# Performance work log

Measured on AMD Instinct MI355X. Metric: run time of the kernel, lower is better.

The kernel has to match this reference:

```python
import jax, jax.numpy as jnp
import numpy as np

K = 10  # hardcoded top-k in the original forward


def setup_inputs() -> dict:
    key = jax.random.key(0)
    ks = jax.random.split(key, 7)
    B, F, N = 192, 256, 512
    stdv = 1.0 / np.sqrt(F)
    return {
        "v": jax.random.normal(ks[0], (B, F, N), dtype=jnp.float32),
        "g_w": jax.random.normal(ks[1], (F, F), dtype=jnp.float32) * stdv,  # Conv1d k=1 weight [out,in]
        "g_b": jax.random.normal(ks[2], (F,), dtype=jnp.float32) * stdv,
        "w1": jax.random.uniform(ks[3], (F, F), jnp.float32, -stdv, stdv),
        "b1": jax.random.uniform(ks[4], (F,), jnp.float32, -stdv, stdv),
        "w2": jax.random.uniform(ks[5], (F, F), jnp.float32, -stdv, stdv),
        "b2": jax.random.uniform(ks[6], (F,), jnp.float32, -stdv, stdv),
    }


def reference(v, g_w, g_b, w1, b1, w2, b2):
    B, Fdim, N = v.shape
    # g: Conv1d(k=1) then permute -> [B, N, nhid]
    g_v = jnp.einsum('bfn,hf->bnh', v, g_w) + g_b
    # affinity A = v^T v : [B, N, N]
    A = jnp.einsum('bfn,bfm->bnm', v, v)
    # top-K sparsification: keep only top-K entries per row
    _, idx = jax.lax.top_k(A, K)  # [B, N, K]
    b_i = jnp.arange(B)[:, None, None]
    n_i = jnp.arange(N)[None, :, None]
    keep = jnp.zeros(A.shape, dtype=bool).at[b_i, n_i, idx].set(True)
    A = jnp.where(keep, A, jnp.zeros((), A.dtype))
    # add self loops
    A = A + jnp.eye(N, dtype=A.dtype)
    # D^-0.5 A D^-0.5 (diagonal scaling, equivalent to diag_embed matmuls)
    deg = jnp.sum(A, axis=-1)  # [B, N]
    d = deg ** -0.5
    d = jnp.where(jnp.isinf(d), jnp.zeros((), d.dtype), d)
    A_hat = d[:, :, None] * A * d[:, None, :]
    # GCN layer 1: relu(A_hat @ (g_v @ w1) + b1)  (dropout p=0 -> identity)
    x = jax.nn.relu(jnp.einsum('bnm,bmh->bnh', A_hat, g_v @ w1) + b1)
    # GCN layer 2
    x = jnp.einsum('bnm,bmh->bnh', A_hat, x @ w2) + b2
    # permute back and residual
    return jnp.transpose(x, (0, 2, 1)) + v
```

## Files before the change

kernel.cpp:

```cpp
#include <hip/hip_runtime.h>
#include <float.h>

#define F_DIM 256
#define N_DIM 512
#define B_DIM 192
#define K_TOP 10

typedef __attribute__((ext_vector_type(8))) short short8;
typedef __attribute__((ext_vector_type(4))) float f32x4;

__device__ inline unsigned short f2bf(float x) {
    unsigned u = __builtin_bit_cast(unsigned, x);
    return (unsigned short)((u + 0x7fffu + ((u >> 16) & 1u)) >> 16);
}

__global__ __launch_bounds__(256) void k_combine(const float* __restrict__ g_w,
                                                 const float* __restrict__ g_b,
                                                 const float* __restrict__ w1,
                                                 const float* __restrict__ w2,
                                                 unsigned short* __restrict__ Wt1,
                                                 float* __restrict__ bc,
                                                 unsigned short* __restrict__ W2t) {
    const int j = threadIdx.x;
    const int bx = blockIdx.x;
    if (bx < F_DIM) {
        float acc = 0.f;
        for (int h = 0; h < F_DIM; ++h) acc += g_w[h * F_DIM + bx] * w1[h * F_DIM + j];
        Wt1[j * F_DIM + bx] = f2bf(acc);
    } else if (bx == F_DIM) {
        float acc = 0.f;
        for (int h = 0; h < F_DIM; ++h) acc += g_b[h] * w1[h * F_DIM + j];
        bc[j] = acc;
    } else {
        int f = bx - F_DIM - 1;
        W2t[j * F_DIM + f] = f2bf(w2[f * F_DIM + j]);
    }
}

__global__ __launch_bounds__(256) void k_to_bf16t(const float* __restrict__ v,
                                                  unsigned short* __restrict__ vt) {
    __shared__ float tile[32][33];
    const int b = blockIdx.z;
    const int n0 = blockIdx.x * 32;
    const int f0 = blockIdx.y * 32;
    const int tx = threadIdx.x & 31, ty = threadIdx.x >> 5;
    const float* vb = v + (size_t)b * F_DIM * N_DIM;
#pragma unroll
    for (int q = 0; q < 4; ++q)
        tile[ty + q * 8][tx] = vb[(size_t)(f0 + ty + q * 8) * N_DIM + n0 + tx];
    __syncthreads();
    const int wn = threadIdx.x >> 4;
    const int wf = threadIdx.x & 15;
    unsigned* vt32 = (unsigned*)vt;
#pragma unroll
    for (int q2 = 0; q2 < 2; ++q2) {
        int row = wn + q2 * 16;
        unsigned lo = f2bf(tile[wf * 2][row]);
        unsigned hi = f2bf(tile[wf * 2 + 1][row]);
        vt32[(size_t)(b * N_DIM + n0 + row) * (F_DIM / 2) + (f0 >> 1) + wf] = lo | (hi << 16);
    }
}

__global__ __launch_bounds__(256, 2) void k_topk_reg(const unsigned short* __restrict__ vt,
                                                     float* __restrict__ deg,
                                                     int* __restrict__ idxb,
                                                     float* __restrict__ wb) {
    __shared__ unsigned short stage[2][N_DIM * 32];

    const int lid = blockIdx.y * 8 + blockIdx.x;
    const int slot = lid >> 3;
    const int b = (lid & 7) + 8 * (slot >> 3);
    const int nblk = slot & 7;

    const int w = threadIdx.x >> 6;
    const int l = threadIdx.x & 63;
    const int l15 = l & 15;
    const int g = l >> 4;
    const int n0w = nblk * 64 + w * 16;
    const unsigned short* vtb = vt + (size_t)b * N_DIM * F_DIM;

    short8 bf[8];
#pragma unroll
    for (int s = 0; s < 8; ++s)
        bf[s] = *(const short8*)(vtb + (size_t)(n0w + l15) * F_DIM + s * 32 + g * 8);

    f32x4 acc[32];
#pragma unroll
    for (int mt = 0; mt < 32; ++mt) acc[mt] = (f32x4){0.f, 0.f, 0.f, 0.f};

#define STAGE(c, bufi)                                                           \
    {                                                                            \
        _Pragma("unroll")                                                        \
        for (int k = 0; k < 8; ++k) {                                            \
            int sid = w * 512 + k * 64 + l;                                      \
            int row = sid >> 2;                                                  \
            int sl = sid & 3;                                                    \
            const unsigned short* src = vtb + (size_t)row * F_DIM + (c) * 32 +   \
                                        ((sl ^ ((row >> 1) & 3)) << 3);          \
            __builtin_amdgcn_global_load_lds(                                    \
                (const __attribute__((address_space(1))) void*)src,              \
                (__attribute__((address_space(3))) void*)(                       \
                    (char*)&stage[bufi][0] + (size_t)(w * 512 + k * 64) * 16),   \
                16, 0, 0);                                                       \
        }                                                                        \
    }

    STAGE(0, 0);
    asm volatile("s_waitcnt vmcnt(0)" ::: "memory");
    __syncthreads();

    const int slx = g ^ ((l15 >> 1) & 3);
    for (int c = 0; c < 8; ++c) {
        const int cur = c & 1;
        if (c < 7) STAGE(c + 1, cur ^ 1);
        const char* sb = (const char*)&stage[cur][0];
        short8 bcur = bf[c];
#pragma unroll
        for (int mt = 0; mt < 32; ++mt) {
            const int row = mt * 16 + l15;
            short8 a = *(const short8*)(sb + row * 64 + (slx << 4));
            acc[mt] = __builtin_amdgcn_mfma_f32_16x16x32_bf16(a, bcur, acc[mt], 0, 0, 0);
        }
        asm volatile("s_waitcnt vmcnt(0)" ::: "memory");
        __syncthreads();
    }
#undef STAGE

    const int row = b * N_DIM + n0w + l15;
    float sum = 0.f;
    for (int it = 0; it < K_TOP; ++it) {
        float chv[4]; int che[4];
#pragma unroll
        for (int c = 0; c < 4; ++c) {
            float tv[16]; int te[16];
#pragma unroll
            for (int p = 0; p < 16; ++p) {
                const int e0 = c * 32 + 2 * p, e1 = e0 + 1;
                float a = acc[e0 >> 2][e0 & 3];
                float bb2 = acc[e1 >> 2][e1 & 3];
                bool tk = bb2 > a;
                tv[p] = tk ? bb2 : a;
                te[p] = tk ? e1 : e0;
            }
#pragma unroll
            for (int len = 8; len >= 1; len >>= 1) {
#pragma unroll
                for (int i2 = 0; i2 < 8; ++i2) {
                    if (i2 < len) {
                        bool tk = tv[i2 + len] > tv[i2];
                        tv[i2] = tk ? tv[i2 + len] : tv[i2];
                        te[i2] = tk ? te[i2 + len] : te[i2];
                    }
                }
            }
            chv[c] = tv[0]; che[c] = te[0];
        }
        bool t1 = chv[1] > chv[0];
        float m0 = t1 ? chv[1] : chv[0]; int ea = t1 ? che[1] : che[0];
        bool t2 = chv[3] > chv[2];
        float m1 = t2 ? chv[3] : chv[2]; int eb = t2 ? che[3] : che[2];
        bool t3 = m1 > m0;
        float bv = t3 ? m1 : m0; int be = t3 ? eb : ea;
        int bm = ((be >> 2) << 4) | (g << 2) | (be & 3);

#pragma unroll
        for (int off = 16; off <= 32; off <<= 1) {
            float ov = __shfl_xor(bv, off, 64);
            int om = __shfl_xor(bm, off, 64);
            if (ov > bv || (ov == bv && om < bm)) { bv = ov; bm = om; }
        }
        sum += bv;
        if (l < 16) {
            idxb[row * K_TOP + it] = bm;
            wb[row * (K_TOP + 1) + it] = bv;
        }
        if (it < K_TOP - 1) {
            int eo = ((bm >> 4) << 2) | (bm & 3);
            eo = (((bm >> 2) & 3) == g) ? eo : 999;
#pragma unroll
            for (int e = 0; e < 128; ++e)
                acc[e >> 2][e & 3] = (e == eo) ? -FLT_MAX : acc[e >> 2][e & 3];
        }
    }
    if (l < 16) deg[row] = sum + 1.0f;
}

template <bool ADD_BIAS>
__global__ __launch_bounds__(256, 2) void k_gemm_mfma(const unsigned short* __restrict__ At,
                                                      const unsigned short* __restrict__ Wt,
                                                      const float* __restrict__ bias,
                                                      float* __restrict__ C) {
    const int b = blockIdx.y;
    const int w = threadIdx.x >> 6;
    const int l = threadIdx.x & 63;
    const int l15 = l & 15;
    const int g = l >> 4;
    const int n0w = blockIdx.x * 128 + w * 32;
    const unsigned short* Ab = At + (size_t)b * N_DIM * F_DIM;

    f32x4 acc0[16], acc1[16];
#pragma unroll
    for (int jt = 0; jt < 16; ++jt) {
        acc0[jt] = (f32x4){0.f, 0.f, 0.f, 0.f};
        acc1[jt] = (f32x4){0.f, 0.f, 0.f, 0.f};
    }

    for (int s = 0; s < 8; ++s) {
        short8 a0 = *(const short8*)(Ab + (size_t)(n0w + l15) * F_DIM + s * 32 + g * 8);
        short8 a1 = *(const short8*)(Ab + (size_t)(n0w + 16 + l15) * F_DIM + s * 32 + g * 8);
#pragma unroll
        for (int jt = 0; jt < 16; ++jt) {
            short8 bf = *(const short8*)(Wt + (size_t)(jt * 16 + l15) * F_DIM + s * 32 + g * 8);
            acc0[jt] = __builtin_amdgcn_mfma_f32_16x16x32_bf16(a0, bf, acc0[jt], 0, 0, 0);
            acc1[jt] = __builtin_amdgcn_mfma_f32_16x16x32_bf16(a1, bf, acc1[jt], 0, 0, 0);
        }
    }

#pragma unroll
    for (int jt = 0; jt < 16; ++jt) {
        float bv = ADD_BIAS ? bias[jt * 16 + l15] : 0.f;
#pragma unroll
        for (int q = 0; q < 4; ++q) {
            int r0 = n0w + g * 4 + q;
            C[((size_t)b * N_DIM + r0) * F_DIM + jt * 16 + l15] = acc0[jt][q] + bv;
            int r1 = n0w + 16 + g * 4 + q;
            C[((size_t)b * N_DIM + r1) * F_DIM + jt * 16 + l15] = acc1[jt][q] + bv;
        }
    }
}

__global__ __launch_bounds__(256) void k_spmm_bf16(const float* __restrict__ X,
                                                   const int* __restrict__ idxb,
                                                   const float* __restrict__ wbr,
                                                   const float* __restrict__ deg,
                                                   const float* __restrict__ bias,
                                                   unsigned short* __restrict__ Y) {
    const int lid = blockIdx.x;
    const int slot = lid >> 3;
    const int b = (lid & 7) + 8 * (slot >> 7);
    const int rowblk = slot & 127;
    const int w = threadIdx.x >> 6;
    const int l = threadIdx.x & 63;
    const int row = b * N_DIM + rowblk * 4 + w;

    const float* Xb = X + ((size_t)b << 9) * F_DIM;
    const float* degb = deg + b * N_DIM;
    const int* id = idxb + row * K_TOP;
    const float* raw = wbr + row * (K_TOP + 1);

    const float dgs = deg[row];
    const float dn = (dgs == 0.f) ? 0.f : 1.f / sqrtf(dgs);
    float4 bv = ((const float4*)bias)[l];
    float4 xv = ((const float4*)(X + (size_t)row * F_DIM))[l];
    const float ws = dn * dn;
    float4 acc;
    acc.x = ws * xv.x + bv.x; acc.y = ws * xv.y + bv.y;
    acc.z = ws * xv.z + bv.z; acc.w = ws * xv.w + bv.w;
#pragma unroll
    for (int i = 0; i < K_TOP; ++i) {
        int m = id[i];
        float dgm = degb[m];
        float dm = (dgm == 0.f) ? 0.f : 1.f / sqrtf(dgm);
        float wi = dn * raw[i] * dm;
        float4 gv = ((const float4*)(Xb + ((size_t)m << 8)))[l];
        acc.x += wi * gv.x; acc.y += wi * gv.y;
        acc.z += wi * gv.z; acc.w += wi * gv.w;
    }
    acc.x = fmaxf(acc.x, 0.f); acc.y = fmaxf(acc.y, 0.f);
    acc.z = fmaxf(acc.z, 0.f); acc.w = fmaxf(acc.w, 0.f);
    uint2 p;
    p.x = (unsigned)f2bf(acc.x) | ((unsigned)f2bf(acc.y) << 16);
    p.y = (unsigned)f2bf(acc.z) | ((unsigned)f2bf(acc.w) << 16);
    ((uint2*)Y)[(size_t)row * (F_DIM / 4) + l] = p;
}

__global__ __launch_bounds__(256) void k_spmm_trans(const float* __restrict__ X,
                                                    const int* __restrict__ idxb,
                                                    const float* __restrict__ wbr,
                                                    const float* __restrict__ deg,
                                                    const float* __restrict__ bias,
                                                    const float* __restrict__ v,
                                                    float* __restrict__ out) {
    __shared__ float tile[32][257];
    const int lid = blockIdx.x;
    const int slot = lid >> 3;
    const int b = (lid & 7) + 8 * (slot >> 4);
    const int n0 = (slot & 15) * 32;
    const int w = threadIdx.x >> 6;
    const int l = threadIdx.x & 63;

    const float* Xb = X + ((size_t)b << 9) * F_DIM;
    const float* degb = deg + b * N_DIM;
    float4 bv = ((const float4*)bias)[l];

    for (int r8 = 0; r8 < 8; ++r8) {
        const int rloc = w * 8 + r8;
        const int row = b * N_DIM + n0 + rloc;
        const int* id = idxb + row * K_TOP;
        const float* raw = wbr + row * (K_TOP + 1);
        const float dgs = deg[row];
        const float dn = (dgs == 0.f) ? 0.f : 1.f / sqrtf(dgs);
        float4 xv = ((const float4*)(X + (size_t)row * F_DIM))[l];
        const float ws = dn * dn;
        float4 acc;
        acc.x = ws * xv.x + bv.x; acc.y = ws * xv.y + bv.y;
        acc.z = ws * xv.z + bv.z; acc.w = ws * xv.w + bv.w;
#pragma unroll
        for (int i = 0; i < K_TOP; ++i) {
            int m = id[i];
            float dgm = degb[m];
            float dm = (dgm == 0.f) ? 0.f : 1.f / sqrtf(dgm);
            float wi = dn * raw[i] * dm;
            float4 gv = ((const float4*)(Xb + ((size_t)m << 8)))[l];
            acc.x += wi * gv.x; acc.y += wi * gv.y;
            acc.z += wi * gv.z; acc.w += wi * gv.w;
        }
        tile[rloc][l * 4 + 0] = acc.x;
        tile[rloc][l * 4 + 1] = acc.y;
        tile[rloc][l * 4 + 2] = acc.z;
        tile[rloc][l * 4 + 3] = acc.w;
    }
    __syncthreads();

    const int i8 = l & 7;
    const int j8 = l >> 3;
#pragma unroll
    for (int k = 0; k < 8; ++k) {
        const int f = (k * 4 + w) * 8 + j8;
        const size_t vo = (size_t)b * F_DIM * N_DIM + (size_t)f * N_DIM + n0;
        float4 vv = ((const float4*)(v + vo))[i8];
        float4 o;
        o.x = tile[i8 * 4 + 0][f] + vv.x;
        o.y = tile[i8 * 4 + 1][f] + vv.y;
        o.z = tile[i8 * 4 + 2][f] + vv.z;
        o.w = tile[i8 * 4 + 3][f] + vv.w;
        ((float4*)(out + vo))[i8] = o;
    }
}

extern "C" void kernel_launch(void* const* d_in, const int* in_sizes, int n_in,
                              void* d_out, int out_size, void* d_ws, size_t ws_size,
                              hipStream_t stream) {
    const float* v   = (const float*)d_in[0];
    const float* g_w = (const float*)d_in[1];
    const float* g_b = (const float*)d_in[2];
    const float* w1  = (const float*)d_in[3];
    const float* b1  = (const float*)d_in[4];
    const float* w2  = (const float*)d_in[5];
    const float* b2  = (const float*)d_in[6];
    float* out = (float*)d_out;

    const size_t S = (size_t)B_DIM * N_DIM * F_DIM;
    float* bufA = (float*)d_ws;
    float* bufB = bufA + S;
    float* bc   = bufB + S;
    float* deg  = bc + F_DIM;
    float* wb   = deg + (size_t)B_DIM * N_DIM;
    int*   idxb = (int*)(wb + (size_t)B_DIM * N_DIM * (K_TOP + 1));
    unsigned short* Wt1 = (unsigned short*)(idxb + (size_t)B_DIM * N_DIM * K_TOP);
    unsigned short* W2t = Wt1 + F_DIM * F_DIM;

    unsigned short* vt   = (unsigned short*)bufB;
    unsigned short* x1bf = (unsigned short*)bufB;

    k_combine<<<dim3(2 * F_DIM + 2), 256, 0, stream>>>(g_w, g_b, w1, w2, Wt1, bc, W2t);
    k_to_bf16t<<<dim3(N_DIM / 32, F_DIM / 32, B_DIM), 256, 0, stream>>>(v, vt);
    k_topk_reg<<<dim3(N_DIM / 64, B_DIM), 256, 0, stream>>>(vt, deg, idxb, wb);
    k_gemm_mfma<true><<<dim3(N_DIM / 128, B_DIM), 256, 0, stream>>>(vt, Wt1, bc, bufA);
    k_spmm_bf16<<<dim3(B_DIM * N_DIM / 4), 256, 0, stream>>>(bufA, idxb, wb, deg, b1, x1bf);
    k_gemm_mfma<false><<<dim3(N_DIM / 128, B_DIM), 256, 0, stream>>>(x1bf, W2t, nullptr, bufA);
    k_spmm_trans<<<dim3(B_DIM * N_DIM / 32), 256, 0, stream>>>(bufA, idxb, wb, deg, b2, v, out);
}
```

Measured before the change: 546.1 us.

## Precompute normalized edge weights once and halve transpose tile in output SpMM

Adds a small kernel that computes the D^-1/2 A D^-1/2 edge weights and self-loop weight per row once, storing them in a padded 12-float buffer. Both SpMM kernels then read the precomputed weights instead of gathering neighbor degrees and computing rsqrt twice. The final transpose kernel now processes its 32 rows in two passes of 16 with a smaller shared tile, which lowers LDS use and may raise occupancy. The cost is an extra launch plus one more global write and read of the weight buffer, which sits in the unused upper half of bufB.

Result: faster. 510.4 us (-6.5%).

```diff
diff --git a/kernel.cpp b/kernel.cpp
--- a/kernel.cpp
+++ b/kernel.cpp
@@ -185,6 +185,24 @@
     if (l < 16) deg[row] = sum + 1.0f;
 }
 
+__global__ __launch_bounds__(256) void k_scale(const float* __restrict__ deg,
+                                               const int* __restrict__ idxb,
+                                               const float* __restrict__ wb,
+                                               float* __restrict__ wbs) {
+    const int row = blockIdx.x * 256 + threadIdx.x;
+    const float dg = deg[row];
+    const float dn = (dg == 0.f) ? 0.f : 1.f / sqrtf(dg);
+    const int bb = (row >> 9) << 9;
+#pragma unroll
+    for (int i = 0; i < K_TOP; ++i) {
+        int m = idxb[row * K_TOP + i];
+        float dgm = deg[bb + m];
+        float dm = (dgm == 0.f) ? 0.f : 1.f / sqrtf(dgm);
+        wbs[row * 12 + i] = dn * wb[row * (K_TOP + 1) + i] * dm;
+    }
+    wbs[row * 12 + K_TOP] = dn * dn;
+}
+
 template <bool ADD_BIAS>
 __global__ __launch_bounds__(256, 2) void k_gemm_mfma(const unsigned short* __restrict__ At,
                                                       const unsigned short* __restrict__ Wt,
@@ -231,8 +249,7 @@
 
 __global__ __launch_bounds__(256) void k_spmm_bf16(const float* __restrict__ X,
                                                    const int* __restrict__ idxb,
-                                                   const float* __restrict__ wbr,
-                                                   const float* __restrict__ deg,
+                                                   const float* __restrict__ wbs,
                                                    const float* __restrict__ bias,
                                                    unsigned short* __restrict__ Y) {
     const int lid = blockIdx.x;
@@ -244,25 +261,19 @@
     const int row = b * N_DIM + rowblk * 4 + w;
 
     const float* Xb = X + ((size_t)b << 9) * F_DIM;
-    const float* degb = deg + b * N_DIM;
     const int* id = idxb + row * K_TOP;
-    const float* raw = wbr + row * (K_TOP + 1);
-
-    const float dgs = deg[row];
-    const float dn = (dgs == 0.f) ? 0.f : 1.f / sqrtf(dgs);
+    const float* ww = wbs + (size_t)row * 12;
+
     float4 bv = ((const float4*)bias)[l];
     float4 xv = ((const float4*)(X + (size_t)row * F_DIM))[l];
-    const float ws = dn * dn;
+    const float ws = ww[K_TOP];
     float4 acc;
     acc.x = ws * xv.x + bv.x; acc.y = ws * xv.y + bv.y;
     acc.z = ws * xv.z + bv.z; acc.w = ws * xv.w + bv.w;
 #pragma unroll
     for (int i = 0; i < K_TOP; ++i) {
-        int m = id[i];
-        float dgm = degb[m];
-        float dm = (dgm == 0.f) ? 0.f : 1.f / sqrtf(dgm);
-        float wi = dn * raw[i] * dm;
-        float4 gv = ((const float4*)(Xb + ((size_t)m << 8)))[l];
+        float wi = ww[i];
+        float4 gv = ((const float4*)(Xb + ((size_t)id[i] << 8)))[l];
         acc.x += wi * gv.x; acc.y += wi * gv.y;
         acc.z += wi * gv.z; acc.w += wi * gv.w;
     }
@@ -276,12 +287,11 @@
 
 __global__ __launch_bounds__(256) void k_spmm_trans(const float* __restrict__ X,
                                                     const int* __restrict__ idxb,
-                                                    const float* __restrict__ wbr,
-                                                    const float* __restrict__ deg,
+                                                    const float* __restrict__ wbs,
                                                     const float* __restrict__ bias,
                                                     const float* __restrict__ v,
                                                     float* __restrict__ out) {
-    __shared__ float tile[32][257];
+    __shared__ float tile[16][260];
     const int lid = blockIdx.x;
     const int slot = lid >> 3;
     const int b = (lid & 7) + 8 * (slot >> 4);
@@ -290,51 +300,47 @@
     const int l = threadIdx.x & 63;
 
     const float* Xb = X + ((size_t)b << 9) * F_DIM;
-    const float* degb = deg + b * N_DIM;
     float4 bv = ((const float4*)bias)[l];
-
-    for (int r8 = 0; r8 < 8; ++r8) {
-        const int rloc = w * 8 + r8;
-        const int row = b * N_DIM + n0 + rloc;
-        const int* id = idxb + row * K_TOP;
-        const float* raw = wbr + row * (K_TOP + 1);
-        const float dgs = deg[row];
-        const float dn = (dgs == 0.f) ? 0.f : 1.f / sqrtf(dgs);
-        float4 xv = ((const float4*)(X + (size_t)row * F_DIM))[l];
-        const float ws = dn * dn;
-        float4 acc;
-        acc.x = ws * xv.x + bv.x; acc.y = ws * xv.y + bv.y;
-        acc.z = ws * xv.z + bv.z; acc.w = ws * xv.w + bv.w;
-#pragma unroll
-        for (int i = 0; i < K_TOP; ++i) {
-            int m = id[i];
-            float dgm = degb[m];
-            float dm = (dgm == 0.f) ? 0.f : 1.f / sqrtf(dgm);
-            float wi = dn * raw[i] * dm;
-            float4 gv = ((const float4*)(Xb + ((size_t)m << 8)))[l];
-            acc.x += wi * gv.x; acc.y += wi * gv.y;
-            acc.z += wi * gv.z; acc.w += wi * gv.w;
-        }
-        tile[rloc][l * 4 + 0] = acc.x;
-        tile[rloc][l * 4 + 1] = acc.y;
-        tile[rloc][l * 4 + 2] = acc.z;
-        tile[rloc][l * 4 + 3] = acc.w;
-    }
-    __syncthreads();
-
-    const int i8 = l & 7;
-    const int j8 = l >> 3;
-#pragma unroll
-    for (int k = 0; k < 8; ++k) {
-        const int f = (k * 4 + w) * 8 + j8;
-        const size_t vo = (size_t)b * F_DIM * N_DIM + (size_t)f * N_DIM + n0;
-        float4 vv = ((const float4*)(v + vo))[i8];
-        float4 o;
-        o.x = tile[i8 * 4 + 0][f] + vv.x;
-        o.y = tile[i8 * 4 + 1][f] + vv.y;
-        o.z = tile[i8 * 4 + 2][f] + vv.z;
-        o.w = tile[i8 * 4 + 3][f] + vv.w;
-        ((float4*)(out + vo))[i8] = o;
+    const int i4 = l & 3, fj = l >> 2;
+
+    for (int p = 0; p < 2; ++p) {
+        if (p) __syncthreads();
+#pragma unroll
+        for (int r4 = 0; r4 < 4; ++r4) {
+            const int rloc = w * 4 + r4;
+            const int row = b * N_DIM + n0 + p * 16 + rloc;
+            const int* id = idxb + row * K_TOP;
+            const float* ww = wbs + (size_t)row * 12;
+            float4 xv = ((const float4*)(X + (size_t)row * F_DIM))[l];
+            const float ws = ww[K_TOP];
+            float4 acc;
+            acc.x = ws * xv.x + bv.x; acc.y = ws * xv.y + bv.y;
+            acc.z = ws * xv.z + bv.z; acc.w = ws * xv.w + bv.w;
+#pragma unroll
+            for (int i = 0; i < K_TOP; ++i) {
+                float wi = ww[i];
+                float4 gv = ((const float4*)(Xb + ((size_t)id[i] << 8)))[l];
+                acc.x += wi * gv.x; acc.y += wi * gv.y;
+                acc.z += wi * gv.z; acc.w += wi * gv.w;
+            }
+            tile[rloc][l * 4 + 0] = acc.x;
+            tile[rloc][l * 4 + 1] = acc.y;
+            tile[rloc][l * 4 + 2] = acc.z;
+            tile[rloc][l * 4 + 3] = acc.w;
+        }
+        __syncthreads();
+#pragma unroll
+        for (int k = 0; k < 4; ++k) {
+            const int f = k * 64 + w * 16 + fj;
+            const size_t vo = (size_t)b * F_DIM * N_DIM + (size_t)f * N_DIM + n0 + p * 16;
+            float4 vv = ((const float4*)(v + vo))[i4];
+            float4 o;
+            o.x = tile[i4 * 4 + 0][f] + vv.x;
+            o.y = tile[i4 * 4 + 1][f] + vv.y;
+            o.z = tile[i4 * 4 + 2][f] + vv.z;
+            o.w = tile[i4 * 4 + 3][f] + vv.w;
+            ((float4*)(out + vo))[i4] = o;
+        }
     }
 }
 
@@ -362,12 +368,14 @@
 
     unsigned short* vt   = (unsigned short*)bufB;
     unsigned short* x1bf = (unsigned short*)bufB;
+    float* wbs = bufB + S / 2;
 
     k_combine<<<dim3(2 * F_DIM + 2), 256, 0, stream>>>(g_w, g_b, w1, w2, Wt1, bc, W2t);
     k_to_bf16t<<<dim3(N_DIM / 32, F_DIM / 32, B_DIM), 256, 0, stream>>>(v, vt);
     k_topk_reg<<<dim3(N_DIM / 64, B_DIM), 256, 0, stream>>>(vt, deg, idxb, wb);
+    k_scale<<<dim3(B_DIM * N_DIM / 256), 256, 0, stream>>>(deg, idxb, wb, wbs);
     k_gemm_mfma<true><<<dim3(N_DIM / 128, B_DIM), 256, 0, stream>>>(vt, Wt1, bc, bufA);
-    k_spmm_bf16<<<dim3(B_DIM * N_DIM / 4), 256, 0, stream>>>(bufA, idxb, wb, deg, b1, x1bf);
+    k_spmm_bf16<<<dim3(B_DIM * N_DIM / 4), 256, 0, stream>>>(bufA, idxb, wbs, b1, x1bf);
     k_gemm_mfma<false><<<dim3(N_DIM / 128, B_DIM), 256, 0, stream>>>(x1bf, W2t, nullptr, bufA);
-    k_spmm_trans<<<dim3(B_DIM * N_DIM / 32), 256, 0, stream>>>(bufA, idxb, wb, deg, b2, v, out);
-}
+    k_spmm_trans<<<dim3(B_DIM * N_DIM / 32), 256, 0, stream>>>(bufA, idxb, wbs, b2, v, out);
+}
```
